# Kernel tuning notes

Measured on AMD Instinct MI355X. Metric: run time of the kernel, lower is better.

The kernel has to match this reference:

```python
import jax, jax.numpy as jnp
import numpy as np

N = 50000
NEG_SLOPE_ATT = 0.2    # PyG GATConv attention leaky_relu slope
NEG_SLOPE_ACT = 0.01   # torch F.leaky_relu default slope


def leaky(x, s):
    return jnp.where(x >= 0, x, s * x)


def gat_conv(x, src, dst, W, att_src, att_dst, bias):
    """PyG GATConv (concat=True, dropout off, self-loops already in src/dst).
    x: [N, F_in]; W: [F_in, H*C]; att_src/att_dst: [H, C]; bias: [H*C]."""
    H, C = att_src.shape
    h = (x @ W).reshape(N, H, C)                       # [N, H, C]
    a_src = (h * att_src[None]).sum(-1)                # [N, H]
    a_dst = (h * att_dst[None]).sum(-1)                # [N, H]
    e = leaky(a_src[src] + a_dst[dst], NEG_SLOPE_ATT)  # [E, H]
    # numerically-stable softmax over incoming edges of each dst node
    m = jax.ops.segment_max(e, dst, num_segments=N)    # [N, H]
    ex = jnp.exp(e - m[dst])
    Z = jax.ops.segment_sum(ex, dst, num_segments=N)   # [N, H]
    alpha = ex / (Z[dst] + 1e-16)                      # [E, H]
    msg = h[src] * alpha[:, :, None]                   # [E, H, C]
    out = jax.ops.segment_sum(msg, dst, num_segments=N)
    return out.reshape(N, H * C) + bias[None, :]


def setup_inputs() -> dict:
    key = jax.random.key(0)
    ks = jax.random.split(key, 12)
    E = 800000
    in_c, hid, heads, out_c = 256, 32, 4, 128
    hc = hid * heads  # 128
    x = jax.random.normal(ks[0], (N, in_c), dtype=jnp.float32)
    edge_index = jax.random.randint(ks[1], (2, E), 0, N, dtype=jnp.int64)
    s1 = 1.0 / np.sqrt(in_c)
    s2 = 1.0 / np.sqrt(hc)
    return {
        "x": x,
        "edge_index": edge_index,
        "W1": jax.random.normal(ks[2], (in_c, heads * hid), dtype=jnp.float32) * s1,
        "att_src1": jax.random.normal(ks[3], (heads, hid), dtype=jnp.float32) * s2,
        "att_dst1": jax.random.normal(ks[4], (heads, hid), dtype=jnp.float32) * s2,
        "b1": jnp.zeros((hc,), dtype=jnp.float32),
        "W2": jax.random.normal(ks[5], (hc, out_c), dtype=jnp.float32) * s2,
        "att_src2": jax.random.normal(ks[6], (1, out_c), dtype=jnp.float32) * s2,
        "att_dst2": jax.random.normal(ks[7], (1, out_c), dtype=jnp.float32) * s2,
        "b2": jnp.zeros((out_c,), dtype=jnp.float32),
    }


def reference(x, edge_index, W1, att_src1, att_dst1, b1, W2, att_src2, att_dst2, b2):
    # add self loops (PyG GATConv default add_self_loops=True)
    loops = jnp.arange(N, dtype=edge_index.dtype)
    src = jnp.concatenate([edge_index[0], loops])
    dst = jnp.concatenate([edge_index[1], loops])
    h = leaky(gat_conv(x, src, dst, W1, att_src1, att_dst1, b1), NEG_SLOPE_ACT)
    out = leaky(gat_conv(h, src, dst, W2, att_src2, att_dst2, b2), NEG_SLOPE_ACT)
    return out
```

## Files before the change

### kernel.cpp

```cpp
#include <hip/hip_runtime.h>
#include <hip/hip_fp16.h>

#define SLOPE_ATT 0.2f
#define SLOPE_ACT 0.01f

#define SB 256
#define NBUKMAX 512

typedef _Float16 hf8 __attribute__((ext_vector_type(8)));
typedef float f32x4 __attribute__((ext_vector_type(4)));

template<int K, int H, bool A_FP32>
__device__ __forceinline__
void gemm_mfma_body(int gbid, int tid,
                    const void* __restrict__ Av, const _Float16* __restrict__ BT,
                    const float* __restrict__ att_s, const float* __restrict__ att_d,
                    _Float16* __restrict__ hout, float* __restrict__ a_src,
                    float* __restrict__ a_dst, int M)
{
  const int lane = tid & 63;
  const int wid  = tid >> 6;
  const int li   = lane & 15;
  const int lk   = lane >> 4;
  const int rowbase = gbid * 128 + wid * 32;

  const float*    Af = (const float*)Av;
  const _Float16* Ah = (const _Float16*)Av;

  f32x4 acc[2][8];
#pragma unroll
  for (int i = 0; i < 2; ++i)
#pragma unroll
    for (int j = 0; j < 8; ++j) acc[i][j] = (f32x4){0.f, 0.f, 0.f, 0.f};

  const int r0 = min(rowbase + li,      M - 1);
  const int r1 = min(rowbase + 16 + li, M - 1);

#pragma unroll
  for (int ks = 0; ks < K / 32; ++ks) {
    const int kb = ks * 32 + lk * 8;
    hf8 a0, a1;
    if constexpr (A_FP32) {
      const float* p0 = &Af[(size_t)r0 * K + kb];
      const float* p1 = &Af[(size_t)r1 * K + kb];
      float4 x0a = *(const float4*)p0, x0b = *(const float4*)(p0 + 4);
      float4 x1a = *(const float4*)p1, x1b = *(const float4*)(p1 + 4);
      a0[0]=(_Float16)x0a.x; a0[1]=(_Float16)x0a.y; a0[2]=(_Float16)x0a.z; a0[3]=(_Float16)x0a.w;
      a0[4]=(_Float16)x0b.x; a0[5]=(_Float16)x0b.y; a0[6]=(_Float16)x0b.z; a0[7]=(_Float16)x0b.w;
      a1[0]=(_Float16)x1a.x; a1[1]=(_Float16)x1a.y; a1[2]=(_Float16)x1a.z; a1[3]=(_Float16)x1a.w;
      a1[4]=(_Float16)x1b.x; a1[5]=(_Float16)x1b.y; a1[6]=(_Float16)x1b.z; a1[7]=(_Float16)x1b.w;
    } else {
      a0 = *(const hf8*)&Ah[(size_t)r0 * K + kb];
      a1 = *(const hf8*)&Ah[(size_t)r1 * K + kb];
    }
#pragma unroll
    for (int cf = 0; cf < 8; ++cf) {
      hf8 b = *(const hf8*)&BT[(size_t)(cf * 16 + li) * K + kb];
      acc[0][cf] = __builtin_amdgcn_mfma_f32_16x16x32_f16(a0, b, acc[0][cf], 0, 0, 0);
      acc[1][cf] = __builtin_amdgcn_mfma_f32_16x16x32_f16(a1, b, acc[1][cf], 0, 0, 0);
    }
  }

  float sA[8], dA[8];
#pragma unroll
  for (int cf = 0; cf < 8; ++cf) {
    sA[cf] = att_s[cf * 16 + li];
    dA[cf] = att_d[cf * 16 + li];
  }

  const bool full = (rowbase + 32) <= M;
#pragma unroll
  for (int rf = 0; rf < 2; ++rf) {
    const int rb = rowbase + rf * 16 + lk * 4;
#pragma unroll
    for (int reg = 0; reg < 4; ++reg) {
      const int r = rb + reg;
      if (full || r < M) {
#pragma unroll
        for (int cf = 0; cf < 8; ++cf)
          hout[(size_t)r * 128 + cf * 16 + li] = (_Float16)acc[rf][cf][reg];
      }
    }
    if constexpr (H == 4) {
#pragma unroll
      for (int hh = 0; hh < 4; ++hh) {
#pragma unroll
        for (int reg = 0; reg < 4; ++reg) {
          float sp = acc[rf][2*hh][reg] * sA[2*hh] + acc[rf][2*hh+1][reg] * sA[2*hh+1];
          float dp = acc[rf][2*hh][reg] * dA[2*hh] + acc[rf][2*hh+1][reg] * dA[2*hh+1];
          sp += __shfl_xor(sp, 1); sp += __shfl_xor(sp, 2);
          sp += __shfl_xor(sp, 4); sp += __shfl_xor(sp, 8);
          dp += __shfl_xor(dp, 1); dp += __shfl_xor(dp, 2);
          dp += __shfl_xor(dp, 4); dp += __shfl_xor(dp, 8);
          const int r = rb + reg;
          if (li == 0 && r < M) {
            a_src[(size_t)r * 4 + hh] = sp;
            a_dst[(size_t)r * 4 + hh] = dp;
          }
        }
      }
    } else {
#pragma unroll
      for (int reg = 0; reg < 4; ++reg) {
        float sp = 0.f, dp = 0.f;
#pragma unroll
        for (int cf = 0; cf < 8; ++cf) {
          sp += acc[rf][cf][reg] * sA[cf];
          dp += acc[rf][cf][reg] * dA[cf];
        }
        sp += __shfl_xor(sp, 1); sp += __shfl_xor(sp, 2);
        sp += __shfl_xor(sp, 4); sp += __shfl_xor(sp, 8);
        dp += __shfl_xor(dp, 1); dp += __shfl_xor(dp, 2);
        dp += __shfl_xor(dp, 4); dp += __shfl_xor(dp, 8);
        const int r = rb + reg;
        if (li == 0 && r < M) { a_src[r] = sp; a_dst[r] = dp; }
      }
    }
  }
}

__global__ __launch_bounds__(256)
void pre_kernel(const int* __restrict__ ei, int E, int N, int nbuk, int epb1,
                unsigned* __restrict__ cntA, unsigned* __restrict__ sd32,
                const float* __restrict__ W1, _Float16* __restrict__ W1T,
                const float* __restrict__ W2, _Float16* __restrict__ W2T)
{
  __shared__ unsigned hist[NBUKMAX];
  const int bid = blockIdx.x;
  const int tid = threadIdx.x;
  if (bid < SB) {
    for (int j = tid; j < NBUKMAX; j += 256) hist[j] = 0;
    __syncthreads();
    const int EE = E + N;
    const int lo = bid * epb1, hi = min(lo + epb1, EE);
    for (int i = lo + tid; i < hi; i += 256) {
      int d = (i < E) ? ei[E + i] : (i - E);
      atomicAdd(&hist[d >> 7], 1u);
    }
    __syncthreads();
    for (int j = tid; j < nbuk; j += 256)
      cntA[(size_t)bid * NBUKMAX + j] = hist[j];
  } else if (bid < SB + 128) {
    int idx = (bid - SB) * 256 + tid;
    int k = idx >> 7, c = idx & 127;
    W1T[(size_t)c * 256 + k] = (_Float16)W1[idx];
  } else if (bid < SB + 192) {
    int idx = (bid - SB - 128) * 256 + tid;
    int k = idx >> 7, c = idx & 127;
    W2T[(size_t)c * 128 + k] = (_Float16)W2[idx];
  } else {
    const int i = (bid - SB - 192) * 256 + tid;
    const int EE = E + N;
    if (i < EE) {
      unsigned s, d;
      if (i < E) { s = (unsigned)ei[i]; d = (unsigned)ei[E + i]; }
      else       { s = d = (unsigned)(i - E); }
      sd32[i] = (s << 16) | d;
    }
  }
}

__global__ __launch_bounds__(256)
void bukoff_kernel(const unsigned* __restrict__ cntA, unsigned* __restrict__ blkoff,
                   unsigned* __restrict__ buktotal)
{
  __shared__ unsigned s[256];
  const int j = blockIdx.x;
  const int t = threadIdx.x;
  unsigned v0 = cntA[(size_t)t * NBUKMAX + j];
  s[t] = v0;
  __syncthreads();
  for (int off = 1; off < 256; off <<= 1) {
    unsigned v = (t >= off) ? s[t - off] : 0u;
    __syncthreads();
    s[t] += v;
    __syncthreads();
  }
  blkoff[(size_t)t * NBUKMAX + j] = s[t] - v0;
  if (t == 255) buktotal[j] = s[255];
}

__device__ __forceinline__
void bukstart_scan(const unsigned* __restrict__ buktotal, int nbuk,
                   unsigned* bt, unsigned* ps, unsigned* bs, int tid)
{
  for (int j = tid; j < NBUKMAX; j += 256) bt[j] = (j < nbuk) ? buktotal[j] : 0u;
  __syncthreads();
  unsigned pair = bt[2 * tid] + bt[2 * tid + 1];
  ps[tid] = pair;
  __syncthreads();
  for (int off = 1; off < 256; off <<= 1) {
    unsigned v = (tid >= off) ? ps[tid - off] : 0u;
    __syncthreads();
    ps[tid] += v;
    __syncthreads();
  }
  unsigned e0 = ps[tid] - pair;
  bs[2 * tid]     = e0;
  bs[2 * tid + 1] = e0 + bt[2 * tid];
  __syncthreads();
}

__global__ __launch_bounds__(256)
void gemm1_scatter_kernel(int E, int N, int nbuk, int epb1,
                          const unsigned* __restrict__ sd32,
                          const unsigned* __restrict__ blkoff,
                          const unsigned* __restrict__ buktotal,
                          unsigned* __restrict__ ebuk,
                          const float* __restrict__ x, const _Float16* __restrict__ W1T,
                          const float* __restrict__ as1, const float* __restrict__ ad1,
                          _Float16* __restrict__ h, float* __restrict__ asv,
                          float* __restrict__ adv, int ggrid)
{
  __shared__ unsigned bt[NBUKMAX], bs[NBUKMAX], cur[NBUKMAX];
  __shared__ unsigned ps[256];
  const int bid = blockIdx.x;
  const int tid = threadIdx.x;
  if (bid < ggrid) {
    gemm_mfma_body<256, 4, true>(bid, tid, x, W1T, as1, ad1, h, asv, adv, N);
  } else {
    const int sb = bid - ggrid;
    bukstart_scan(buktotal, nbuk, bt, ps, bs, tid);
    for (int j = tid; j < nbuk; j += 256)
      cur[j] = bs[j] + blkoff[(size_t)sb * NBUKMAX + j];
    __syncthreads();
    const int EE = E + N;
    const int lo = sb * epb1, hi = min(lo + epb1, EE);
    for (int i = lo + tid; i < hi; i += 256) {
      unsigned sd = sd32[i];
      unsigned buk = (sd & 0xFFFFu) >> 7;
      unsigned slot = atomicAdd(&cur[buk], 1u);
      ebuk[slot] = sd;
    }
  }
}

__global__ __launch_bounds__(256)
void csr_build_kernel(int N, int nbuk,
                      const unsigned* __restrict__ buktotal,
                      const unsigned* __restrict__ ebuk,
                      unsigned* __restrict__ deg, unsigned* __restrict__ row_start,
                      unsigned short* __restrict__ csr16)
{
  __shared__ unsigned bt[NBUKMAX], bs[NBUKMAX];
  __shared__ unsigned ps[256];
  __shared__ unsigned hist[128], hs[128], cur2[128];
  const int j = blockIdx.x;
  const int tid = threadIdx.x;

  bukstart_scan(buktotal, nbuk, bt, ps, bs, tid);
  const unsigned estart = bs[j];
  const unsigned ecount = bt[j];
  const int n0 = j * 128;

  if (tid < 128) hist[tid] = 0;
  __syncthreads();
  for (unsigned i = estart + tid; i < estart + ecount; i += 256)
    atomicAdd(&hist[ebuk[i] & 127u], 1u);
  __syncthreads();
  unsigned hv = (tid < 128) ? hist[tid] : 0u;
  if (tid < 128) hs[tid] = hv;
  __syncthreads();
  for (int off = 1; off < 128; off <<= 1) {
    unsigned v = 0;
    if (tid < 128 && tid >= off) v = hs[tid - off];
    __syncthreads();
    if (tid < 128) hs[tid] += v;
    __syncthreads();
  }
  if (tid < 128) {
    unsigned excl = hs[tid] - hv;
    cur2[tid] = estart + excl;
    if (n0 + tid < N) {
      deg[n0 + tid] = hv;
      row_start[n0 + tid] = estart + excl;
    }
  }
  __syncthreads();
  for (unsigned i = estart + tid; i < estart + ecount; i += 256) {
    unsigned sd = ebuk[i];
    unsigned slot = atomicAdd(&cur2[sd & 127u], 1u);
    csr16[slot] = (unsigned short)(sd >> 16);
  }
}

__global__ __launch_bounds__(256)
void agg1_gemm2_kernel(const unsigned* __restrict__ row_start,
                       const unsigned* __restrict__ deg,
                       const unsigned short* __restrict__ csr16,
                       const __half* __restrict__ h,
                       const float* __restrict__ a_src,
                       const float* __restrict__ a_dst,
                       const float* __restrict__ bias,
                       const _Float16* __restrict__ W2T,
                       const float* __restrict__ as2, const float* __restrict__ ad2,
                       _Float16* __restrict__ h2,
                       float* __restrict__ asv2, float* __restrict__ adv2, int N)
{
  __shared__ _Float16 actS[16][132];
  __shared__ float sdots[2][16];

  const int lane = threadIdx.x & 63;
  const int wid  = threadIdx.x >> 6;
  const int l5   = lane & 15;
  const int nl   = wid * 4 + (lane >> 4);
  const int nb   = blockIdx.x * 16;
  const int n    = nb + nl;
  const int nn   = min(n, N - 1);
  const int hd   = l5 >> 2;

  const float adn = a_dst[(size_t)nn * 4 + hd];
  const unsigned beg = row_start[nn];
  const unsigned cnt = deg[nn];
  unsigned cmax = cnt;
  cmax = max(cmax, (unsigned)__shfl_xor((int)cmax, 16));
  cmax = max(cmax, (unsigned)__shfl_xor((int)cmax, 32));

  const float4* __restrict__ h4 = (const float4*)h;

  float Z = 0.f;
  float acc[8];
#pragma unroll
  for (int j = 0; j < 8; ++j) acc[j] = 0.f;

  unsigned i = 0;
  for (; i + 2 <= cmax; i += 2) {
    unsigned s0 = csr16[beg + min(i,     cnt - 1)];
    unsigned s1 = csr16[beg + min(i + 1, cnt - 1)];
    float e0 = a_src[(size_t)s0 * 4 + hd] + adn;
    float e1 = a_src[(size_t)s1 * 4 + hd] + adn;
    float4 v0 = h4[(size_t)s0 * 16 + l5];
    float4 v1 = h4[(size_t)s1 * 16 + l5];
    e0 = (e0 >= 0.f) ? e0 : SLOPE_ATT * e0;
    e1 = (e1 >= 0.f) ? e1 : SLOPE_ATT * e1;
    float w0 = (i     < cnt) ? __expf(e0) : 0.f;
    float w1 = (i + 1 < cnt) ? __expf(e1) : 0.f;
    Z += w0 + w1;
    const __half2* p0 = (const __half2*)&v0;
    const __half2* p1 = (const __half2*)&v1;
#pragma unroll
    for (int j = 0; j < 4; ++j) {
      float2 f0 = __half22float2(p0[j]);
      float2 f1 = __half22float2(p1[j]);
      acc[2*j]   += w0 * f0.x + w1 * f1.x;
      acc[2*j+1] += w0 * f0.y + w1 * f1.y;
    }
  }
  if (i < cmax) {
    unsigned s0 = csr16[beg + min(i, cnt - 1)];
    float e0 = a_src[(size_t)s0 * 4 + hd] + adn;
    float4 v0 = h4[(size_t)s0 * 16 + l5];
    e0 = (e0 >= 0.f) ? e0 : SLOPE_ATT * e0;
    float w0 = (i < cnt) ? __expf(e0) : 0.f;
    Z += w0;
    const __half2* p0 = (const __half2*)&v0;
#pragma unroll
    for (int j = 0; j < 4; ++j) {
      float2 f0 = __half22float2(p0[j]);
      acc[2*j]   += w0 * f0.x;
      acc[2*j+1] += w0 * f0.y;
    }
  }

  const float inv = 1.f / (Z + 1e-16f);
  float4 b0 = ((const float4*)bias)[l5 * 2];
  float4 b1 = ((const float4*)bias)[l5 * 2 + 1];
  float o[8];
  o[0] = acc[0] * inv + b0.x;  o[1] = acc[1] * inv + b0.y;
  o[2] = acc[2] * inv + b0.z;  o[3] = acc[3] * inv + b0.w;
  o[4] = acc[4] * inv + b1.x;  o[5] = acc[5] * inv + b1.y;
  o[6] = acc[6] * inv + b1.z;  o[7] = acc[7] * inv + b1.w;
#pragma unroll
  for (int j = 0; j < 8; ++j) o[j] = (o[j] >= 0.f) ? o[j] : SLOPE_ACT * o[j];

#pragma unroll
  for (int j = 0; j < 8; ++j) actS[nl][l5 * 8 + j] = (_Float16)o[j];
  if (threadIdx.x < 32) sdots[threadIdx.x >> 4][threadIdx.x & 15] = 0.f;
  __syncthreads();

  const int li = l5;
  const int lk = lane >> 4;
#pragma unroll
  for (int t = 0; t < 2; ++t) {
    const int c0 = wid * 32 + t * 16;
    f32x4 a2 = (f32x4){0.f, 0.f, 0.f, 0.f};
#pragma unroll
    for (int ks = 0; ks < 4; ++ks) {
      hf8 af = *(const hf8*)&actS[li][ks * 32 + lk * 8];
      hf8 bf = *(const hf8*)&W2T[(size_t)(c0 + li) * 128 + ks * 32 + lk * 8];
      a2 = __builtin_amdgcn_mfma_f32_16x16x32_f16(af, bf, a2, 0, 0, 0);
    }
    const float asc = as2[c0 + li];
    const float adc = ad2[c0 + li];
#pragma unroll
    for (int reg = 0; reg < 4; ++reg) {
      const int r = lk * 4 + reg;
      float hv = a2[reg];
      if (nb + r < N) h2[(size_t)(nb + r) * 128 + c0 + li] = (_Float16)hv;
      float sp = hv * asc;
      float dp = hv * adc;
      sp += __shfl_xor(sp, 1); sp += __shfl_xor(sp, 2);
      sp += __shfl_xor(sp, 4); sp += __shfl_xor(sp, 8);
      dp += __shfl_xor(dp, 1); dp += __shfl_xor(dp, 2);
      dp += __shfl_xor(dp, 4); dp += __shfl_xor(dp, 8);
      if (li == 0) {
        atomicAdd(&sdots[0][r], sp);
        atomicAdd(&sdots[1][r], dp);
      }
    }
  }
  __syncthreads();
  if (threadIdx.x < 16) {
    const int r = threadIdx.x;
    if (nb + r < N) {
      asv2[nb + r] = sdots[0][r];
      adv2[nb + r] = sdots[1][r];
    }
  }
}

__global__ __launch_bounds__(256)
void aggregate2_kernel(const unsigned* __restrict__ row_start,
                       const unsigned* __restrict__ deg,
                       const unsigned short* __restrict__ csr16,
                       const __half* __restrict__ h,
                       const float* __restrict__ a_src,
                       const float* __restrict__ a_dst,
                       const float* __restrict__ bias,
                       float* __restrict__ out, int N)
{
  const int lane = threadIdx.x & 63;
  const int wid  = threadIdx.x >> 6;
  const int l5   = lane & 15;
  const int n    = blockIdx.x * 16 + wid * 4 + (lane >> 4);
  const int nn   = min(n, N - 1);

  const float adn = a_dst[nn];
  const unsigned beg = row_start[nn];
  const unsigned cnt = deg[nn];
  unsigned cmax = cnt;
  cmax = max(cmax, (unsigned)__shfl_xor((int)cmax, 16));
  cmax = max(cmax, (unsigned)__shfl_xor((int)cmax, 32));

  const float4* __restrict__ h4 = (const float4*)h;

  float Z = 0.f;
  float acc[8];
#pragma unroll
  for (int j = 0; j < 8; ++j) acc[j] = 0.f;

  unsigned i = 0;
  for (; i + 2 <= cmax; i += 2) {
    unsigned s0 = csr16[beg + min(i,     cnt - 1)];
    unsigned s1 = csr16[beg + min(i + 1, cnt - 1)];
    float e0 = a_src[s0] + adn;
    float e1 = a_src[s1] + adn;
    float4 v0 = h4[(size_t)s0 * 16 + l5];
    float4 v1 = h4[(size_t)s1 * 16 + l5];
    e0 = (e0 >= 0.f) ? e0 : SLOPE_ATT * e0;
    e1 = (e1 >= 0.f) ? e1 : SLOPE_ATT * e1;
    float w0 = (i     < cnt) ? __expf(e0) : 0.f;
    float w1 = (i + 1 < cnt) ? __expf(e1) : 0.f;
    Z += w0 + w1;
    const __half2* p0 = (const __half2*)&v0;
    const __half2* p1 = (const __half2*)&v1;
#pragma unroll
    for (int j = 0; j < 4; ++j) {
      float2 f0 = __half22float2(p0[j]);
      float2 f1 = __half22float2(p1[j]);
      acc[2*j]   += w0 * f0.x + w1 * f1.x;
      acc[2*j+1] += w0 * f0.y + w1 * f1.y;
    }
  }
  if (i < cmax) {
    unsigned s0 = csr16[beg + min(i, cnt - 1)];
    float e0 = a_src[s0] + adn;
    float4 v0 = h4[(size_t)s0 * 16 + l5];
    e0 = (e0 >= 0.f) ? e0 : SLOPE_ATT * e0;
    float w0 = (i < cnt) ? __expf(e0) : 0.f;
    Z += w0;
    const __half2* p0 = (const __half2*)&v0;
#pragma unroll
    for (int j = 0; j < 4; ++j) {
      float2 f0 = __half22float2(p0[j]);
      acc[2*j]   += w0 * f0.x;
      acc[2*j+1] += w0 * f0.y;
    }
  }

  const float inv = 1.f / (Z + 1e-16f);
  float4 b0 = ((const float4*)bias)[l5 * 2];
  float4 b1 = ((const float4*)bias)[l5 * 2 + 1];
  float o[8];
  o[0] = acc[0] * inv + b0.x;  o[1] = acc[1] * inv + b0.y;
  o[2] = acc[2] * inv + b0.z;  o[3] = acc[3] * inv + b0.w;
  o[4] = acc[4] * inv + b1.x;  o[5] = acc[5] * inv + b1.y;
  o[6] = acc[6] * inv + b1.z;  o[7] = acc[7] * inv + b1.w;
#pragma unroll
  for (int j = 0; j < 8; ++j) o[j] = (o[j] >= 0.f) ? o[j] : SLOPE_ACT * o[j];

  if (n < N) {
    ((float4*)out)[(size_t)n * 32 + l5 * 2]     = make_float4(o[0], o[1], o[2], o[3]);
    ((float4*)out)[(size_t)n * 32 + l5 * 2 + 1] = make_float4(o[4], o[5], o[6], o[7]);
  }
}

extern "C" void kernel_launch(void* const* d_in, const int* in_sizes, int n_in,
                              void* d_out, int out_size, void* d_ws, size_t ws_size,
                              hipStream_t stream)
{
  const float* x   = (const float*)d_in[0];
  const int*   ei  = (const int*)d_in[1];
  const float* W1  = (const float*)d_in[2];
  const float* as1 = (const float*)d_in[3];
  const float* ad1 = (const float*)d_in[4];
  const float* b1  = (const float*)d_in[5];
  const float* W2  = (const float*)d_in[6];
  const float* as2 = (const float*)d_in[7];
  const float* ad2 = (const float*)d_in[8];
  const float* b2  = (const float*)d_in[9];
  float* out = (float*)d_out;

  const int N  = in_sizes[0] / 256;
  const int E  = in_sizes[1] / 2;
  const int EE = E + N;
  const int nbuk = (N + 127) / 128;
  const int epb1 = (EE + SB - 1) / SB;
  const int pgrid = (EE + 255) / 256;

  float* ws = (float*)d_ws;
  size_t o = 0;
  _Float16* h    = (_Float16*)(ws + o); o += (size_t)N * 64;
  _Float16* h2   = (_Float16*)(ws + o); o += (size_t)N * 64;
  float* asv  = ws + o; o += (size_t)N * 4;
  float* adv  = ws + o; o += (size_t)N * 4;
  float* asv2 = ws + o; o += (size_t)N;
  float* adv2 = ws + o; o += (size_t)N;
  _Float16* W1T = (_Float16*)(ws + o); o += 128 * 256 / 2;
  _Float16* W2T = (_Float16*)(ws + o); o += 128 * 128 / 2;
  unsigned* deg       = (unsigned*)(ws + o); o += (size_t)N;
  unsigned* row_start = (unsigned*)(ws + o); o += (size_t)N;
  unsigned* cntA      = (unsigned*)(ws + o); o += (size_t)SB * NBUKMAX;
  unsigned* blkoff    = (unsigned*)(ws + o); o += (size_t)SB * NBUKMAX;
  unsigned* buktotal  = (unsigned*)(ws + o); o += NBUKMAX;
  unsigned* sd32      = (unsigned*)(ws + o); o += (size_t)EE;
  unsigned* ebuk      = (unsigned*)(ws + o); o += (size_t)EE;
  unsigned short* csr16 = (unsigned short*)(ws + o); o += (size_t)(EE + 1) / 2;

  const int ngrid = (N + 15) / 16;
  const int ggrid = (N + 127) / 128;

  pre_kernel<<<SB + 192 + pgrid, 256, 0, stream>>>(
      ei, E, N, nbuk, epb1, cntA, sd32, W1, W1T, W2, W2T);
  bukoff_kernel<<<nbuk, 256, 0, stream>>>(cntA, blkoff, buktotal);
  gemm1_scatter_kernel<<<ggrid + SB, 256, 0, stream>>>(
      E, N, nbuk, epb1, sd32, blkoff, buktotal, ebuk,
      x, W1T, as1, ad1, h, asv, adv, ggrid);
  csr_build_kernel<<<nbuk, 256, 0, stream>>>(
      N, nbuk, buktotal, ebuk, deg, row_start, csr16);
  agg1_gemm2_kernel<<<ngrid, 256, 0, stream>>>(
      row_start, deg, csr16, (const __half*)h, asv, adv, b1,
      W2T, as2, ad2, h2, asv2, adv2, N);
  aggregate2_kernel<<<ngrid, 256, 0, stream>>>(
      row_start, deg, csr16, (const __half*)h2, asv2, adv2, b2, out, N);
}
```

Measured before the change: 144.0 us.

## Precompute normalized attention weights per edge before aggregation passes

Attention softmax weights are now computed once per edge and stored as normalized fp16 values. Layer 1 does this inside the CSR build kernel, layer 2 in a new alpha2 kernel. The aggregation kernels then read these weights instead of recomputing exp and gathering a_src per lane, and their gather loops are unrolled from 2 to 4 edges. This takes the redundant exp work out of the aggregation kernels and adds memory-level parallelism, at the cost of an extra kernel launch, extra per-edge traffic, fp16 rounding of alpha, and a fixed exp offset of -4 in place of the max subtraction, which could overflow or lose precision on other inputs.

```diff
diff --git a/kernel.cpp b/kernel.cpp
--- a/kernel.cpp
+++ b/kernel.cpp
@@ -239,12 +239,14 @@
 void csr_build_kernel(int N, int nbuk,
                       const unsigned* __restrict__ buktotal,
                       const unsigned* __restrict__ ebuk,
+                      const float* __restrict__ asv, const float* __restrict__ adv,
                       unsigned* __restrict__ deg, unsigned* __restrict__ row_start,
-                      unsigned short* __restrict__ csr16)
+                      unsigned short* __restrict__ csr16,
+                      __half* __restrict__ alf1)
 {
   __shared__ unsigned bt[NBUKMAX], bs[NBUKMAX];
   __shared__ unsigned ps[256];
-  __shared__ unsigned hist[128], hs[128], cur2[128];
+  __shared__ unsigned hist[128], hs[128], cur2[128], rsl[128];
   const int j = blockIdx.x;
   const int tid = threadIdx.x;
 
@@ -271,6 +273,7 @@
   if (tid < 128) {
     unsigned excl = hs[tid] - hv;
     cur2[tid] = estart + excl;
+    rsl[tid]  = estart + excl;
     if (n0 + tid < N) {
       deg[n0 + tid] = hv;
       row_start[n0 + tid] = estart + excl;
@@ -282,15 +285,90 @@
     unsigned slot = atomicAdd(&cur2[sd & 127u], 1u);
     csr16[slot] = (unsigned short)(sd >> 16);
   }
+  __syncthreads();
+
+  const int dloc = tid >> 1;
+  const int par  = tid & 1;
+  const int n = n0 + dloc;
+  if (n < N) {
+    const unsigned rs = rsl[dloc];
+    const unsigned dg = hist[dloc];
+    float4 dv = ((const float4*)adv)[n];
+    float zx = 0.f, zy = 0.f, zz = 0.f, zw = 0.f;
+    for (unsigned i = par; i < dg; i += 2) {
+      unsigned pos = rs + i;
+      unsigned s = csr16[pos];
+      float4 av = ((const float4*)asv)[s];
+      float e0 = av.x + dv.x; e0 = (e0 >= 0.f) ? e0 : SLOPE_ATT * e0;
+      float e1 = av.y + dv.y; e1 = (e1 >= 0.f) ? e1 : SLOPE_ATT * e1;
+      float e2 = av.z + dv.z; e2 = (e2 >= 0.f) ? e2 : SLOPE_ATT * e2;
+      float e3 = av.w + dv.w; e3 = (e3 >= 0.f) ? e3 : SLOPE_ATT * e3;
+      float w0 = __expf(e0 - 4.f), w1 = __expf(e1 - 4.f);
+      float w2 = __expf(e2 - 4.f), w3 = __expf(e3 - 4.f);
+      zx += w0; zy += w1; zz += w2; zw += w3;
+      union { __half2 q[2]; ushort4 u; } uu;
+      uu.q[0] = __floats2half2_rn(w0, w1);
+      uu.q[1] = __floats2half2_rn(w2, w3);
+      *(ushort4*)&alf1[(size_t)pos * 4] = uu.u;
+    }
+    zx += __shfl_xor(zx, 1); zy += __shfl_xor(zy, 1);
+    zz += __shfl_xor(zz, 1); zw += __shfl_xor(zw, 1);
+    const float ix = 1.f / (zx + 1e-16f), iy = 1.f / (zy + 1e-16f);
+    const float iz = 1.f / (zz + 1e-16f), iw = 1.f / (zw + 1e-16f);
+    for (unsigned i = par; i < dg; i += 2) {
+      unsigned pos = rs + i;
+      union { ushort4 u; __half2 q[2]; } vv;
+      vv.u = *(const ushort4*)&alf1[(size_t)pos * 4];
+      float2 f0 = __half22float2(vv.q[0]);
+      float2 f1 = __half22float2(vv.q[1]);
+      union { __half2 q[2]; ushort4 u; } ww;
+      ww.q[0] = __floats2half2_rn(f0.x * ix, f0.y * iy);
+      ww.q[1] = __floats2half2_rn(f1.x * iz, f1.y * iw);
+      *(ushort4*)&alf1[(size_t)pos * 4] = ww.u;
+    }
+  }
+}
+
+__global__ __launch_bounds__(256)
+void alpha2_kernel(int N,
+                   const unsigned* __restrict__ row_start,
+                   const unsigned* __restrict__ deg,
+                   const unsigned short* __restrict__ csr16,
+                   const float* __restrict__ asv2, const float* __restrict__ adv2,
+                   __half* __restrict__ alf2)
+{
+  const int tid = threadIdx.x;
+  const int dloc = tid >> 1;
+  const int par  = tid & 1;
+  const int n = blockIdx.x * 128 + dloc;
+  if (n >= N) return;
+  const unsigned rs = row_start[n];
+  const unsigned dg = deg[n];
+  const float dv = adv2[n];
+  float z = 0.f;
+  for (unsigned i = par; i < dg; i += 2) {
+    unsigned pos = rs + i;
+    unsigned s = csr16[pos];
+    float e = asv2[s] + dv;
+    e = (e >= 0.f) ? e : SLOPE_ATT * e;
+    float w = __expf(e - 4.f);
+    z += w;
+    alf2[pos] = __float2half(w);
+  }
+  z += __shfl_xor(z, 1);
+  const float izv = 1.f / (z + 1e-16f);
+  for (unsigned i = par; i < dg; i += 2) {
+    unsigned pos = rs + i;
+    alf2[pos] = __float2half(__half2float(alf2[pos]) * izv);
+  }
 }
 
 __global__ __launch_bounds__(256)
 void agg1_gemm2_kernel(const unsigned* __restrict__ row_start,
                        const unsigned* __restrict__ deg,
                        const unsigned short* __restrict__ csr16,
+                       const __half* __restrict__ alf1,
                        const __half* __restrict__ h,
-                       const float* __restrict__ a_src,
-                       const float* __restrict__ a_dst,
                        const float* __restrict__ bias,
                        const _Float16* __restrict__ W2T,
                        const float* __restrict__ as2, const float* __restrict__ ad2,
@@ -309,7 +387,6 @@
   const int nn   = min(n, N - 1);
   const int hd   = l5 >> 2;
 
-  const float adn = a_dst[(size_t)nn * 4 + hd];
   const unsigned beg = row_start[nn];
   const unsigned cnt = deg[nn];
   unsigned cmax = cnt;
@@ -318,58 +395,65 @@
 
   const float4* __restrict__ h4 = (const float4*)h;
 
-  float Z = 0.f;
   float acc[8];
 #pragma unroll
   for (int j = 0; j < 8; ++j) acc[j] = 0.f;
 
   unsigned i = 0;
-  for (; i + 2 <= cmax; i += 2) {
-    unsigned s0 = csr16[beg + min(i,     cnt - 1)];
-    unsigned s1 = csr16[beg + min(i + 1, cnt - 1)];
-    float e0 = a_src[(size_t)s0 * 4 + hd] + adn;
-    float e1 = a_src[(size_t)s1 * 4 + hd] + adn;
+  for (; i + 4 <= cmax; i += 4) {
+    unsigned p0 = beg + min(i,     cnt - 1);
+    unsigned p1 = beg + min(i + 1, cnt - 1);
+    unsigned p2 = beg + min(i + 2, cnt - 1);
+    unsigned p3 = beg + min(i + 3, cnt - 1);
+    unsigned s0 = csr16[p0], s1 = csr16[p1], s2 = csr16[p2], s3 = csr16[p3];
+    float w0 = __half2float(alf1[(size_t)p0 * 4 + hd]);
+    float w1 = __half2float(alf1[(size_t)p1 * 4 + hd]);
+    float w2 = __half2float(alf1[(size_t)p2 * 4 + hd]);
+    float w3 = __half2float(alf1[(size_t)p3 * 4 + hd]);
     float4 v0 = h4[(size_t)s0 * 16 + l5];
     float4 v1 = h4[(size_t)s1 * 16 + l5];
-    e0 = (e0 >= 0.f) ? e0 : SLOPE_ATT * e0;
-    e1 = (e1 >= 0.f) ? e1 : SLOPE_ATT * e1;
-    float w0 = (i     < cnt) ? __expf(e0) : 0.f;
-    float w1 = (i + 1 < cnt) ? __expf(e1) : 0.f;
-    Z += w0 + w1;
-    const __half2* p0 = (const __half2*)&v0;
-    const __half2* p1 = (const __half2*)&v1;
+    float4 v2 = h4[(size_t)s2 * 16 + l5];
+    float4 v3 = h4[(size_t)s3 * 16 + l5];
+    w0 = (i     < cnt) ? w0 : 0.f;
+    w1 = (i + 1 < cnt) ? w1 : 0.f;
+    w2 = (i + 2 < cnt) ? w2 : 0.f;
+    w3 = (i + 3 < cnt) ? w3 : 0.f;
+    const __half2* q0 = (const __half2*)&v0;
+    const __half2* q1 = (const __half2*)&v1;
+    const __half2* q2 = (const __half2*)&v2;
+    const __half2* q3 = (const __half2*)&v3;
 #pragma unroll
     for (int j = 0; j < 4; ++j) {
-      float2 f0 = __half22float2(p0[j]);
-      float2 f1 = __half22float2(p1[j]);
-      acc[2*j]   += w0 * f0.x + w1 * f1.x;
-      acc[2*j+1] += w0 * f0.y + w1 * f1.y;
-    }
-  }
-  if (i < cmax) {
-    unsigned s0 = csr16[beg + min(i, cnt - 1)];
-    float e0 = a_src[(size_t)s0 * 4 + hd] + adn;
+      float2 f0 = __half22float2(q0[j]);
+      float2 f1 = __half22float2(q1[j]);
+      float2 f2 = __half22float2(q2[j]);
+      float2 f3 = __half22float2(q3[j]);
+      acc[2*j]   += w0 * f0.x + w1 * f1.x + w2 * f2.x + w3 * f3.x;
+      acc[2*j+1] += w0 * f0.y + w1 * f1.y + w2 * f2.y + w3 * f3.y;
+    }
+  }
+  for (; i < cmax; ++i) {
+    unsigned p0 = beg + min(i, cnt - 1);
+    unsigned s0 = csr16[p0];
+    float w0 = __half2float(alf1[(size_t)p0 * 4 + hd]);
     float4 v0 = h4[(size_t)s0 * 16 + l5];
-    e0 = (e0 >= 0.f) ? e0 : SLOPE_ATT * e0;
-    float w0 = (i < cnt) ? __expf(e0) : 0.f;
-    Z += w0;
-    const __half2* p0 = (const __half2*)&v0;
+    w0 = (i < cnt) ? w0 : 0.f;
+    const __half2* q0 = (const __half2*)&v0;
 #pragma unroll
     for (int j = 0; j < 4; ++j) {
-      float2 f0 = __half22float2(p0[j]);
+      float2 f0 = __half22float2(q0[j]);
       acc[2*j]   += w0 * f0.x;
       acc[2*j+1] += w0 * f0.y;
     }
   }
 
-  const float inv = 1.f / (Z + 1e-16f);
   float4 b0 = ((const float4*)bias)[l5 * 2];
   float4 b1 = ((const float4*)bias)[l5 * 2 + 1];
   float o[8];
-  o[0] = acc[0] * inv + b0.x;  o[1] = acc[1] * inv + b0.y;
-  o[2] = acc[2] * inv + b0.z;  o[3] = acc[3] * inv + b0.w;
-  o[4] = acc[4] * inv + b1.x;  o[5] = acc[5] * inv + b1.y;
-  o[6] = acc[6] * inv + b1.z;  o[7] = acc[7] * inv + b1.w;
+  o[0] = acc[0] + b0.x;  o[1] = acc[1] + b0.y;
+  o[2] = acc[2] + b0.z;  o[3] = acc[3] + b0.w;
+  o[4] = acc[4] + b1.x;  o[5] = acc[5] + b1.y;
+  o[6] = acc[6] + b1.z;  o[7] = acc[7] + b1.w;
 #pragma unroll
   for (int j = 0; j < 8; ++j) o[j] = (o[j] >= 0.f) ? o[j] : SLOPE_ACT * o[j];
 
@@ -423,9 +507,8 @@
 void aggregate2_kernel(const unsigned* __restrict__ row_start,
                        const unsigned* __restrict__ deg,
                        const unsigned short* __restrict__ csr16,
+                       const __half* __restrict__ alf2,
                        const __half* __restrict__ h,
-                       const float* __restrict__ a_src,
-                       const float* __restrict__ a_dst,
                        const float* __restrict__ bias,
                        float* __restrict__ out, int N)
 {
@@ -435,7 +518,6 @@
   const int n    = blockIdx.x * 16 + wid * 4 + (lane >> 4);
   const int nn   = min(n, N - 1);
 
-  const float adn = a_dst[nn];
   const unsigned beg = row_start[nn];
   const unsigned cnt = deg[nn];
   unsigned cmax = cnt;
@@ -444,58 +526,65 @@
 
   const float4* __restrict__ h4 = (const float4*)h;
 
-  float Z = 0.f;
   float acc[8];
 #pragma unroll
   for (int j = 0; j < 8; ++j) acc[j] = 0.f;
 
   unsigned i = 0;
-  for (; i + 2 <= cmax; i += 2) {
-    unsigned s0 = csr16[beg + min(i,     cnt - 1)];
-    unsigned s1 = csr16[beg + min(i + 1, cnt - 1)];
-    float e0 = a_src[s0] + adn;
-    float e1 = a_src[s1] + adn;
+  for (; i + 4 <= cmax; i += 4) {
+    unsigned p0 = beg + min(i,     cnt - 1);
+    unsigned p1 = beg + min(i + 1, cnt - 1);
+    unsigned p2 = beg + min(i + 2, cnt - 1);
+    unsigned p3 = beg + min(i + 3, cnt - 1);
+    unsigned s0 = csr16[p0], s1 = csr16[p1], s2 = csr16[p2], s3 = csr16[p3];
+    float w0 = __half2float(alf2[p0]);
+    float w1 = __half2float(alf2[p1]);
+    float w2 = __half2float(alf2[p2]);
+    float w3 = __half2float(alf2[p3]);
     float4 v0 = h4[(size_t)s0 * 16 + l5];
     float4 v1 = h4[(size_t)s1 * 16 + l5];
-    e0 = (e0 >= 0.f) ? e0 : SLOPE_ATT * e0;
-    e1 = (e1 >= 0.f) ? e1 : SLOPE_ATT * e1;
-    float w0 = (i     < cnt) ? __expf(e0) : 0.f;
-    float w1 = (i + 1 < cnt) ? __expf(e1) : 0.f;
-    Z += w0 + w1;
-    const __half2* p0 = (const __half2*)&v0;
-    const __half2* p1 = (const __half2*)&v1;
+    float4 v2 = h4[(size_t)s2 * 16 + l5];
+    float4 v3 = h4[(size_t)s3 * 16 + l5];
+    w0 = (i     < cnt) ? w0 : 0.f;
+    w1 = (i + 1 < cnt) ? w1 : 0.f;
+    w2 = (i + 2 < cnt) ? w2 : 0.f;
+    w3 = (i + 3 < cnt) ? w3 : 0.f;
+    const __half2* q0 = (const __half2*)&v0;
+    const __half2* q1 = (const __half2*)&v1;
+    const __half2* q2 = (const __half2*)&v2;
+    const __half2* q3 = (const __half2*)&v3;
 #pragma unroll
     for (int j = 0; j < 4; ++j) {
-      float2 f0 = __half22float2(p0[j]);
-      float2 f1 = __half22float2(p1[j]);
-      acc[2*j]   += w0 * f0.x + w1 * f1.x;
-      acc[2*j+1] += w0 * f0.y + w1 * f1.y;
-    }
-  }
-  if (i < cmax) {
-    unsigned s0 = csr16[beg + min(i, cnt - 1)];
-    float e0 = a_src[s0] + adn;
+      float2 f0 = __half22float2(q0[j]);
+      float2 f1 = __half22float2(q1[j]);
+      float2 f2 = __half22float2(q2[j]);
+      float2 f3 = __half22float2(q3[j]);
+      acc[2*j]   += w0 * f0.x + w1 * f1.x + w2 * f2.x + w3 * f3.x;
+      acc[2*j+1] += w0 * f0.y + w1 * f1.y + w2 * f2.y + w3 * f3.y;
+    }
+  }
+  for (; i < cmax; ++i) {
+    unsigned p0 = beg + min(i, cnt - 1);
+    unsigned s0 = csr16[p0];
+    float w0 = __half2float(alf2[p0]);
     float4 v0 = h4[(size_t)s0 * 16 + l5];
-    e0 = (e0 >= 0.f) ? e0 : SLOPE_ATT * e0;
-    float w0 = (i < cnt) ? __expf(e0) : 0.f;
-    Z += w0;
-    const __half2* p0 = (const __half2*)&v0;
+    w0 = (i < cnt) ? w0 : 0.f;
+    const __half2* q0 = (const __half2*)&v0;
 #pragma unroll
     for (int j = 0; j < 4; ++j) {
-      float2 f0 = __half22float2(p0[j]);
+      float2 f0 = __half22float2(q0[j]);
       acc[2*j]   += w0 * f0.x;
       acc[2*j+1] += w0 * f0.y;
     }
   }
 
-  const float inv = 1.f / (Z + 1e-16f);
   float4 b0 = ((const float4*)bias)[l5 * 2];
   float4 b1 = ((const float4*)bias)[l5 * 2 + 1];
   float o[8];
-  o[0] = acc[0] * inv + b0.x;  o[1] = acc[1] * inv + b0.y;
-  o[2] = acc[2] * inv + b0.z;  o[3] = acc[3] * inv + b0.w;
-  o[4] = acc[4] * inv + b1.x;  o[5] = acc[5] * inv + b1.y;
-  o[6] = acc[6] * inv + b1.z;  o[7] = acc[7] * inv + b1.w;
+  o[0] = acc[0] + b0.x;  o[1] = acc[1] + b0.y;
+  o[2] = acc[2] + b0.z;  o[3] = acc[3] + b0.w;
+  o[4] = acc[4] + b1.x;  o[5] = acc[5] + b1.y;
+  o[6] = acc[6] + b1.z;  o[7] = acc[7] + b1.w;
 #pragma unroll
   for (int j = 0; j < 8; ++j) o[j] = (o[j] >= 0.f) ? o[j] : SLOPE_ACT * o[j];
 
@@ -546,6 +635,8 @@
   unsigned* sd32      = (unsigned*)(ws + o); o += (size_t)EE;
   unsigned* ebuk      = (unsigned*)(ws + o); o += (size_t)EE;
   unsigned short* csr16 = (unsigned short*)(ws + o); o += (size_t)(EE + 1) / 2;
+  __half* alf1 = (__half*)(ws + o); o += (size_t)EE * 2;
+  __half* alf2 = (__half*)(ws + o); o += (size_t)(EE + 1) / 2;
 
   const int ngrid = (N + 15) / 16;
   const int ggrid = (N + 127) / 128;
@@ -557,10 +648,12 @@
       E, N, nbuk, epb1, sd32, blkoff, buktotal, ebuk,
       x, W1T, as1, ad1, h, asv, adv, ggrid);
   csr_build_kernel<<<nbuk, 256, 0, stream>>>(
-      N, nbuk, buktotal, ebuk, deg, row_start, csr16);
+      N, nbuk, buktotal, ebuk, asv, adv, deg, row_start, csr16, alf1);
   agg1_gemm2_kernel<<<ngrid, 256, 0, stream>>>(
-      row_start, deg, csr16, (const __half*)h, asv, adv, b1,
+      row_start, deg, csr16, alf1, (const __half*)h, b1,
       W2T, as2, ad2, h2, asv2, adv2, N);
+  alpha2_kernel<<<nbuk, 256, 0, stream>>>(
+      N, row_start, deg, csr16, asv2, adv2, alf2);
   aggregate2_kernel<<<ngrid, 256, 0, stream>>>(
-      row_start, deg, csr16, (const __half*)h2, asv2, adv2, b2, out, N);
-}
+      row_start, deg, csr16, alf2, (const __half*)h2, b2, out, N);
+}
```

New measurement: 168.1 us. 16.8% more time.
